# Optimization experiments

Measured on AMD Instinct MI355X. Metric: run time of the kernel, lower is better.

The kernel has to match this reference:

```python
import jax, jax.numpy as jnp
import numpy as np

N_NODES = 50000
N_EDGES = 800000
IN_FEAT = 128
OUT_FEAT = 128


def setup_inputs() -> dict:
    key = jax.random.key(0)
    ks = jax.random.split(key, 12)
    s = lambda fan_in: 1.0 / np.sqrt(fan_in)
    inp = {
        "node_feats": jax.random.normal(ks[0], (N_NODES, IN_FEAT), dtype=jnp.float32),
        "edge_feats": jax.random.normal(ks[1], (N_EDGES, IN_FEAT), dtype=jnp.float32),
        "src": jax.random.randint(ks[2], (N_EDGES,), 0, N_NODES),
        "dst": jax.random.randint(ks[3], (N_EDGES,), 0, N_NODES),
        # mlp1: Linear(2*in -> in), ReLU, Linear(in -> in)
        "W1a": jax.random.uniform(ks[4], (2 * IN_FEAT, IN_FEAT), jnp.float32, -s(2 * IN_FEAT), s(2 * IN_FEAT)),
        "b1a": jnp.zeros((IN_FEAT,), jnp.float32),
        "W1b": jax.random.uniform(ks[5], (IN_FEAT, IN_FEAT), jnp.float32, -s(IN_FEAT), s(IN_FEAT)),
        "b1b": jnp.zeros((IN_FEAT,), jnp.float32),
        # mlp2: Linear(in -> out), ReLU, Linear(out -> out)
        "W2a": jax.random.uniform(ks[6], (IN_FEAT, OUT_FEAT), jnp.float32, -s(IN_FEAT), s(IN_FEAT)),
        "b2a": jnp.zeros((OUT_FEAT,), jnp.float32),
        "W2b": jax.random.uniform(ks[7], (OUT_FEAT, OUT_FEAT), jnp.float32, -s(OUT_FEAT), s(OUT_FEAT)),
        "b2b": jnp.zeros((OUT_FEAT,), jnp.float32),
    }
    return inp


def reference(node_feats, edge_feats, src, dst, W1a, b1a, W1b, b1b, W2a, b2a, W2b, b2b):
    # message: mlp1(cat([h_src, e]))  -> [E, in_feat]
    cat = jnp.concatenate([node_feats[src], edge_feats], axis=1)  # [E, 2*in]
    m = jax.nn.relu(cat @ W1a + b1a) @ W1b + b1b                  # [E, in]
    # reduce: scatter-sum over dst + residual
    agg = jax.ops.segment_sum(m, dst, num_segments=node_feats.shape[0])
    h = agg + node_feats                                          # [N, in]
    # mlp2
    out = jax.nn.relu(h @ W2a + b2a) @ W2b + b2b                  # [N, out]
    return out
```

## Files before the change

### kernel.cpp

```cpp
#include <hip/hip_runtime.h>
#include <hip/hip_bf16.h>

typedef __attribute__((ext_vector_type(8))) short short8;
typedef __attribute__((ext_vector_type(4))) float floatx4;
typedef unsigned short ushort_t;

#define MFMA(a, b, c) __builtin_amdgcn_mfma_f32_16x16x32_bf16((a), (b), (c), 0, 0, 0)

constexpr int N_NODES = 50000;
constexpr int N_EDGES = 800000;
constexpr int EDGE_BLOCKS = N_EDGES / 32;
constexpr int NODE_TILES = (N_NODES + 63) / 64;
constexpr int YS_STRIDE = 136;

__device__ __forceinline__ unsigned short f2b(float x) {
  union { float f; unsigned u; } c; c.f = x;
  unsigned r = c.u + 0x7FFFu + ((c.u >> 16) & 1u);
  return (unsigned short)(r >> 16);
}

__device__ __forceinline__ unsigned pk2(float x, float y) {
  __hip_bfloat162 h = __float22bfloat162_rn(float2{x, y});
  unsigned u; __builtin_memcpy(&u, &h, 4);
  return u;
}

__device__ __forceinline__ short8 mk_frag(const float4 a, const float4 b) {
  union { short8 s; unsigned u[4]; } r;
  r.u[0] = pk2(a.x, a.y); r.u[1] = pk2(a.z, a.w);
  r.u[2] = pk2(b.x, b.y); r.u[3] = pk2(b.z, b.w);
  return r.s;
}

__global__ void prep(const float* __restrict__ W1a, const float* __restrict__ W1b,
                     const float* __restrict__ W2a, const float* __restrict__ W2b,
                     ushort_t* __restrict__ wbuf, float4* __restrict__ agg4) {
  const int t = blockIdx.x * blockDim.x + threadIdx.x;
  const int stride = gridDim.x * blockDim.x;
  const float4 z = {0.f, 0.f, 0.f, 0.f};
  for (int i = t; i < N_NODES * 32; i += stride) agg4[i] = z;

  ushort_t* W1s1 = wbuf;
  ushort_t* W1s2 = wbuf + 32768;
  ushort_t* W2aT = wbuf + 49152;
  ushort_t* W2bT = wbuf + 65536;

  for (int i = t; i < 32768; i += stride) {
    const int j = i & 7, lane = (i >> 3) & 63, fb = i >> 9;
    const int ks = fb >> 3, nt = fb & 7;
    const int k = ks * 32 + (lane >> 4) * 8 + j, n = nt * 16 + (lane & 15);
    W1s1[i] = f2b(W1a[k * 128 + n]);
  }
  for (int i = t; i < 16384; i += stride) {
    const int j = i & 7, lane = (i >> 3) & 63, fb = i >> 9;
    const int ks = fb >> 3, nt = fb & 7;
    const int k = ks * 32 + (lane >> 4) * 8 + j, n = nt * 16 + (lane & 15);
    W1s2[i] = f2b(W1b[k * 128 + n]);
  }
  for (int i = t; i < 16384; i += stride) {
    const int n = i >> 7, k = i & 127;
    W2aT[i] = f2b(W2a[k * 128 + n]);
    W2bT[i] = f2b(W2b[k * 128 + n]);
  }
}

__global__ __launch_bounds__(64, 4) void edge_mlp(
    const float* __restrict__ nf, const float* __restrict__ ef,
    const int* __restrict__ src, const int* __restrict__ dst,
    const float* __restrict__ b1a, const float* __restrict__ b1b,
    const ushort_t* __restrict__ W1s1, const ushort_t* __restrict__ W1s2,
    float* __restrict__ agg) {
  __shared__ __align__(16) ushort_t Ys[32 * YS_STRIDE];

  const int lane = threadIdx.x;
  const int l16 = lane & 15;
  const int quad = lane >> 4;
  const int tb = blockIdx.x * 32;

  const int s0 = src[tb + l16];
  const int s1 = src[tb + 16 + l16];

  floatx4 acc[2][8];
#pragma unroll
  for (int nt = 0; nt < 8; ++nt) {
    const float bz = b1a[nt * 16 + l16];
    acc[0][nt] = (floatx4){bz, bz, bz, bz};
    acc[1][nt] = acc[0][nt];
  }
#pragma unroll
  for (int ks = 0; ks < 8; ++ks) {
    short8 a0, a1;
    if (ks < 4) {
      const float4* p0 = (const float4*)nf + (long)s0 * 32 + ks * 8 + quad * 2;
      const float4* p1 = (const float4*)nf + (long)s1 * 32 + ks * 8 + quad * 2;
      a0 = mk_frag(p0[0], p0[1]);
      a1 = mk_frag(p1[0], p1[1]);
    } else {
      const float4* p0 = (const float4*)ef + (long)(tb + l16) * 32 + (ks - 4) * 8 + quad * 2;
      const float4* p1 = (const float4*)ef + (long)(tb + 16 + l16) * 32 + (ks - 4) * 8 + quad * 2;
      a0 = mk_frag(p0[0], p0[1]);
      a1 = mk_frag(p1[0], p1[1]);
    }
#pragma unroll
    for (int nt = 0; nt < 8; ++nt) {
      const short8 b = *(const short8*)(W1s1 + ((ks * 8 + nt) * 64 + lane) * 8);
      acc[0][nt] = MFMA(a0, b, acc[0][nt]);
      acc[1][nt] = MFMA(a1, b, acc[1][nt]);
    }
  }

#pragma unroll
  for (int mt = 0; mt < 2; ++mt)
#pragma unroll
    for (int nt = 0; nt < 8; ++nt)
#pragma unroll
      for (int r = 0; r < 4; ++r)
        Ys[(mt * 16 + quad * 4 + r) * YS_STRIDE + nt * 16 + l16] =
            f2b(fmaxf(acc[mt][nt][r], 0.f));

  floatx4 acc2[2][8];
#pragma unroll
  for (int nt = 0; nt < 8; ++nt) {
    const float bz = b1b[nt * 16 + l16];
    acc2[0][nt] = (floatx4){bz, bz, bz, bz};
    acc2[1][nt] = acc2[0][nt];
  }
#pragma unroll
  for (int ks = 0; ks < 4; ++ks) {
    const short8 a0 = *(const short8*)(&Ys[l16 * YS_STRIDE + ks * 32 + quad * 8]);
    const short8 a1 = *(const short8*)(&Ys[(16 + l16) * YS_STRIDE + ks * 32 + quad * 8]);
#pragma unroll
    for (int nt = 0; nt < 8; ++nt) {
      const short8 b = *(const short8*)(W1s2 + ((ks * 8 + nt) * 64 + lane) * 8);
      acc2[0][nt] = MFMA(a0, b, acc2[0][nt]);
      acc2[1][nt] = MFMA(a1, b, acc2[1][nt]);
    }
  }

#pragma unroll
  for (int mt = 0; mt < 2; ++mt)
#pragma unroll
    for (int r = 0; r < 4; ++r) {
      const int d = dst[tb + mt * 16 + quad * 4 + r];
      float* base = &agg[(long)d * 128 + l16];
#pragma unroll
      for (int nt = 0; nt < 8; ++nt)
        unsafeAtomicAdd(base + nt * 16, acc2[mt][nt][r]);
    }
}

__global__ __launch_bounds__(256) void node_mlp(
    const float* __restrict__ nf, const float* __restrict__ agg,
    const float* __restrict__ b2a, const float* __restrict__ b2b,
    const ushort_t* __restrict__ W2aT, const ushort_t* __restrict__ W2bT,
    float* __restrict__ out) {
  __shared__ __align__(16) ushort_t Xs[64 * YS_STRIDE];
  __shared__ __align__(16) ushort_t Ys2[64 * YS_STRIDE];

  const int tid = threadIdx.x;
  const int wave = tid >> 6;
  const int lane = tid & 63;
  const int l16 = lane & 15;
  const int quad = lane >> 4;
  const int nbase = wave * 32;
  const int rbase = blockIdx.x * 64;

  short8 bfrA[2][4], bfrB[2][4];
  float biasA[2], biasB[2];
#pragma unroll
  for (int t = 0; t < 2; ++t) {
    const int n = nbase + t * 16 + l16;
#pragma unroll
    for (int ks = 0; ks < 4; ++ks) {
      bfrA[t][ks] = *(const short8*)(W2aT + n * 128 + ks * 32 + quad * 8);
      bfrB[t][ks] = *(const short8*)(W2bT + n * 128 + ks * 32 + quad * 8);
    }
    biasA[t] = b2a[n];
    biasB[t] = b2b[n];
  }

#pragma unroll
  for (int i = 0; i < 8; ++i) {
    const int fidx = tid + 256 * i;
    const int r = fidx >> 5;
    const int c4 = fidx & 31;
    const long gr = min(rbase + r, N_NODES - 1);
    const float4 a = ((const float4*)agg)[gr * 32 + c4];
    const float4 n = ((const float4*)nf)[gr * 32 + c4];
    unsigned* p = (unsigned*)&Xs[r * YS_STRIDE + c4 * 4];
    p[0] = pk2(a.x + n.x, a.y + n.y);
    p[1] = pk2(a.z + n.z, a.w + n.w);
  }
  __syncthreads();

  floatx4 acc[4][2];
#pragma unroll
  for (int mt = 0; mt < 4; ++mt)
#pragma unroll
    for (int t = 0; t < 2; ++t)
      acc[mt][t] = (floatx4){biasA[t], biasA[t], biasA[t], biasA[t]};
#pragma unroll
  for (int ks = 0; ks < 4; ++ks)
#pragma unroll
    for (int mt = 0; mt < 4; ++mt) {
      const short8 a = *(const short8*)(&Xs[(mt * 16 + l16) * YS_STRIDE + ks * 32 + quad * 8]);
      acc[mt][0] = MFMA(a, bfrA[0][ks], acc[mt][0]);
      acc[mt][1] = MFMA(a, bfrA[1][ks], acc[mt][1]);
    }
#pragma unroll
  for (int mt = 0; mt < 4; ++mt)
#pragma unroll
    for (int t = 0; t < 2; ++t)
#pragma unroll
      for (int r = 0; r < 4; ++r) {
        const int row = mt * 16 + quad * 4 + r;
        const int col = nbase + t * 16 + l16;
        Ys2[row * YS_STRIDE + col] = f2b(fmaxf(acc[mt][t][r], 0.f));
      }
  __syncthreads();

  floatx4 acc2[4][2];
#pragma unroll
  for (int mt = 0; mt < 4; ++mt)
#pragma unroll
    for (int t = 0; t < 2; ++t)
      acc2[mt][t] = (floatx4){biasB[t], biasB[t], biasB[t], biasB[t]};
#pragma unroll
  for (int ks = 0; ks < 4; ++ks)
#pragma unroll
    for (int mt = 0; mt < 4; ++mt) {
      const short8 a = *(const short8*)(&Ys2[(mt * 16 + l16) * YS_STRIDE + ks * 32 + quad * 8]);
      acc2[mt][0] = MFMA(a, bfrB[0][ks], acc2[mt][0]);
      acc2[mt][1] = MFMA(a, bfrB[1][ks], acc2[mt][1]);
    }
#pragma unroll
  for (int mt = 0; mt < 4; ++mt)
#pragma unroll
    for (int t = 0; t < 2; ++t)
#pragma unroll
      for (int r = 0; r < 4; ++r) {
        const int row = mt * 16 + quad * 4 + r;
        const int grow = rbase + row;
        if (grow < N_NODES) {
          const int col = nbase + t * 16 + l16;
          out[(long)grow * 128 + col] = acc2[mt][t][r];
        }
      }
}

extern "C" void kernel_launch(void* const* d_in, const int* in_sizes, int n_in,
                              void* d_out, int out_size, void* d_ws, size_t ws_size,
                              hipStream_t stream) {
  const float* nf = (const float*)d_in[0];
  const float* ef = (const float*)d_in[1];
  const int* src = (const int*)d_in[2];
  const int* dst = (const int*)d_in[3];
  const float* W1a = (const float*)d_in[4];
  const float* b1a = (const float*)d_in[5];
  const float* W1b = (const float*)d_in[6];
  const float* b1b = (const float*)d_in[7];
  const float* W2a = (const float*)d_in[8];
  const float* b2a = (const float*)d_in[9];
  const float* W2b = (const float*)d_in[10];
  const float* b2b = (const float*)d_in[11];
  float* out = (float*)d_out;

  char* ws = (char*)d_ws;
  float* agg = (float*)ws;
  ushort_t* wbuf = (ushort_t*)(ws + 25600000);
  const ushort_t* W1s1 = wbuf;
  const ushort_t* W1s2 = wbuf + 32768;
  const ushort_t* W2aT = wbuf + 49152;
  const ushort_t* W2bT = wbuf + 65536;

  prep<<<1024, 256, 0, stream>>>(W1a, W1b, W2a, W2b, wbuf, (float4*)agg);
  edge_mlp<<<EDGE_BLOCKS, 64, 0, stream>>>(nf, ef, src, dst, b1a, b1b, W1s1, W1s2, agg);
  node_mlp<<<NODE_TILES, 256, 0, stream>>>(nf, agg, b2a, b2b, W2aT, W2bT, out);
}
```

Baseline: 1.001 ms.

## Sort edges by destination and pre-reduce messages before atomic scatter

Adds a counting sort of edges by dst (histogram, single-block scan, scatter into a permutation) and has edge_mlp process edges in dst-sorted order. Messages are staged in shared memory and runs of equal dst are summed inside the block, so each run issues one atomic per column instead of one per edge. The sort is meant to cut atomic traffic. In exchange, edge_feats and src are now read as gathers through the permutation rather than streamed, and several extra small kernels run, including a serial one-block scan. The out buffer is reused as scratch for the counts and permutation. Weight fragments are also loaded into registers ahead of each MFMA batch.

Result: faster. 933.8 us (-6.7%).

```diff
diff --git a/kernel.cpp b/kernel.cpp
--- a/kernel.cpp
+++ b/kernel.cpp
@@ -12,6 +12,7 @@
 constexpr int EDGE_BLOCKS = N_EDGES / 32;
 constexpr int NODE_TILES = (N_NODES + 63) / 64;
 constexpr int YS_STRIDE = 136;
+constexpr int MS_STRIDE = 132;
 
 __device__ __forceinline__ unsigned short f2b(float x) {
   union { float f; unsigned u; } c; c.f = x;
@@ -34,11 +35,13 @@
 
 __global__ void prep(const float* __restrict__ W1a, const float* __restrict__ W1b,
                      const float* __restrict__ W2a, const float* __restrict__ W2b,
-                     ushort_t* __restrict__ wbuf, float4* __restrict__ agg4) {
+                     ushort_t* __restrict__ wbuf, float4* __restrict__ agg4,
+                     unsigned* __restrict__ cnt) {
   const int t = blockIdx.x * blockDim.x + threadIdx.x;
   const int stride = gridDim.x * blockDim.x;
   const float4 z = {0.f, 0.f, 0.f, 0.f};
   for (int i = t; i < N_NODES * 32; i += stride) agg4[i] = z;
+  for (int i = t; i < N_NODES; i += stride) cnt[i] = 0u;
 
   ushort_t* W1s1 = wbuf;
   ushort_t* W1s2 = wbuf + 32768;
@@ -64,21 +67,82 @@
   }
 }
 
+__global__ void hist_dst(const int* __restrict__ dst, unsigned* __restrict__ cnt) {
+  int i = blockIdx.x * blockDim.x + threadIdx.x;
+  const int stride = gridDim.x * blockDim.x;
+  for (; i < N_EDGES; i += stride) atomicAdd(&cnt[dst[i]], 1u);
+}
+
+__global__ __launch_bounds__(1024) void scan_cnt(unsigned* __restrict__ cnt) {
+  __shared__ unsigned wsum[16];
+  __shared__ unsigned carry_s;
+  const int tid = threadIdx.x;
+  const int lane = tid & 63, wv = tid >> 6;
+  if (tid == 0) carry_s = 0u;
+  __syncthreads();
+  for (int base = 0; base < N_NODES; base += 1024) {
+    const int i = base + tid;
+    const unsigned v = (i < N_NODES) ? cnt[i] : 0u;
+    unsigned s = v;
+#pragma unroll
+    for (int off = 1; off < 64; off <<= 1) {
+      unsigned t = __shfl_up(s, off);
+      if (lane >= off) s += t;
+    }
+    if (lane == 63) wsum[wv] = s;
+    __syncthreads();
+    if (wv == 0 && lane < 16) {
+      unsigned w = wsum[lane];
+      unsigned sw = w;
+#pragma unroll
+      for (int off = 1; off < 16; off <<= 1) {
+        unsigned t = __shfl_up(sw, off);
+        if (lane >= off) sw += t;
+      }
+      wsum[lane] = sw - w;
+    }
+    __syncthreads();
+    const unsigned excl = s - v + wsum[wv] + carry_s;
+    if (i < N_NODES) cnt[i] = excl;
+    __syncthreads();
+    if (tid == 1023) carry_s = excl + v;
+    __syncthreads();
+  }
+}
+
+__global__ void scatter_idx(const int* __restrict__ dst, unsigned* __restrict__ cnt,
+                            unsigned* __restrict__ perm) {
+  int i = blockIdx.x * blockDim.x + threadIdx.x;
+  const int stride = gridDim.x * blockDim.x;
+  for (; i < N_EDGES; i += stride) {
+    const unsigned pos = atomicAdd(&cnt[dst[i]], 1u);
+    perm[pos] = (unsigned)i;
+  }
+}
+
 __global__ __launch_bounds__(64, 4) void edge_mlp(
     const float* __restrict__ nf, const float* __restrict__ ef,
     const int* __restrict__ src, const int* __restrict__ dst,
+    const unsigned* __restrict__ perm,
     const float* __restrict__ b1a, const float* __restrict__ b1b,
     const ushort_t* __restrict__ W1s1, const ushort_t* __restrict__ W1s2,
     float* __restrict__ agg) {
-  __shared__ __align__(16) ushort_t Ys[32 * YS_STRIDE];
+  __shared__ __align__(16) char smem[32 * MS_STRIDE * 4];
+  ushort_t* Ys = (ushort_t*)smem;
+  float* Ms = (float*)smem;
 
   const int lane = threadIdx.x;
   const int l16 = lane & 15;
   const int quad = lane >> 4;
   const int tb = blockIdx.x * 32;
 
-  const int s0 = src[tb + l16];
-  const int s1 = src[tb + 16 + l16];
+  int dlane = 0;
+  if (lane < 32) dlane = dst[perm[tb + lane]];
+
+  const int e0 = (int)perm[tb + l16];
+  const int e1 = (int)perm[tb + 16 + l16];
+  const int s0 = src[e0];
+  const int s1 = src[e1];
 
   floatx4 acc[2][8];
 #pragma unroll
@@ -96,16 +160,19 @@
       a0 = mk_frag(p0[0], p0[1]);
       a1 = mk_frag(p1[0], p1[1]);
     } else {
-      const float4* p0 = (const float4*)ef + (long)(tb + l16) * 32 + (ks - 4) * 8 + quad * 2;
-      const float4* p1 = (const float4*)ef + (long)(tb + 16 + l16) * 32 + (ks - 4) * 8 + quad * 2;
+      const float4* p0 = (const float4*)ef + (long)e0 * 32 + (ks - 4) * 8 + quad * 2;
+      const float4* p1 = (const float4*)ef + (long)e1 * 32 + (ks - 4) * 8 + quad * 2;
       a0 = mk_frag(p0[0], p0[1]);
       a1 = mk_frag(p1[0], p1[1]);
     }
+    short8 bfr[8];
+#pragma unroll
+    for (int nt = 0; nt < 8; ++nt)
+      bfr[nt] = *(const short8*)(W1s1 + ((ks * 8 + nt) * 64 + lane) * 8);
 #pragma unroll
     for (int nt = 0; nt < 8; ++nt) {
-      const short8 b = *(const short8*)(W1s1 + ((ks * 8 + nt) * 64 + lane) * 8);
-      acc[0][nt] = MFMA(a0, b, acc[0][nt]);
-      acc[1][nt] = MFMA(a1, b, acc[1][nt]);
+      acc[0][nt] = MFMA(a0, bfr[nt], acc[0][nt]);
+      acc[1][nt] = MFMA(a1, bfr[nt], acc[1][nt]);
     }
   }
 
@@ -129,24 +196,39 @@
   for (int ks = 0; ks < 4; ++ks) {
     const short8 a0 = *(const short8*)(&Ys[l16 * YS_STRIDE + ks * 32 + quad * 8]);
     const short8 a1 = *(const short8*)(&Ys[(16 + l16) * YS_STRIDE + ks * 32 + quad * 8]);
+    short8 bfr[8];
+#pragma unroll
+    for (int nt = 0; nt < 8; ++nt)
+      bfr[nt] = *(const short8*)(W1s2 + ((ks * 8 + nt) * 64 + lane) * 8);
 #pragma unroll
     for (int nt = 0; nt < 8; ++nt) {
-      const short8 b = *(const short8*)(W1s2 + ((ks * 8 + nt) * 64 + lane) * 8);
-      acc2[0][nt] = MFMA(a0, b, acc2[0][nt]);
-      acc2[1][nt] = MFMA(a1, b, acc2[1][nt]);
+      acc2[0][nt] = MFMA(a0, bfr[nt], acc2[0][nt]);
+      acc2[1][nt] = MFMA(a1, bfr[nt], acc2[1][nt]);
     }
   }
 
 #pragma unroll
   for (int mt = 0; mt < 2; ++mt)
 #pragma unroll
-    for (int r = 0; r < 4; ++r) {
-      const int d = dst[tb + mt * 16 + quad * 4 + r];
-      float* base = &agg[(long)d * 128 + l16];
-#pragma unroll
-      for (int nt = 0; nt < 8; ++nt)
-        unsafeAtomicAdd(base + nt * 16, acc2[mt][nt][r]);
-    }
+    for (int nt = 0; nt < 8; ++nt)
+#pragma unroll
+      for (int r = 0; r < 4; ++r)
+        Ms[(mt * 16 + quad * 4 + r) * MS_STRIDE + nt * 16 + l16] = acc2[mt][nt][r];
+
+  float a0 = 0.f, a1 = 0.f;
+  int cur = __shfl(dlane, 0);
+  for (int r = 0; r < 32; ++r) {
+    const int d = __shfl(dlane, r);
+    if (d != cur) {
+      unsafeAtomicAdd(&agg[(long)cur * 128 + lane], a0);
+      unsafeAtomicAdd(&agg[(long)cur * 128 + 64 + lane], a1);
+      a0 = 0.f; a1 = 0.f; cur = d;
+    }
+    a0 += Ms[r * MS_STRIDE + lane];
+    a1 += Ms[r * MS_STRIDE + 64 + lane];
+  }
+  unsafeAtomicAdd(&agg[(long)cur * 128 + lane], a0);
+  unsafeAtomicAdd(&agg[(long)cur * 128 + 64 + lane], a1);
 }
 
 __global__ __launch_bounds__(256) void node_mlp(
@@ -273,7 +355,13 @@
   const ushort_t* W2aT = wbuf + 49152;
   const ushort_t* W2bT = wbuf + 65536;
 
-  prep<<<1024, 256, 0, stream>>>(W1a, W1b, W2a, W2b, wbuf, (float4*)agg);
-  edge_mlp<<<EDGE_BLOCKS, 64, 0, stream>>>(nf, ef, src, dst, b1a, b1b, W1s1, W1s2, agg);
+  unsigned* cnt = (unsigned*)out;
+  unsigned* perm = (unsigned*)out + 65536;
+
+  prep<<<1024, 256, 0, stream>>>(W1a, W1b, W2a, W2b, wbuf, (float4*)agg, cnt);
+  hist_dst<<<1024, 256, 0, stream>>>(dst, cnt);
+  scan_cnt<<<1, 1024, 0, stream>>>(cnt);
+  scatter_idx<<<1024, 256, 0, stream>>>(dst, cnt, perm);
+  edge_mlp<<<EDGE_BLOCKS, 64, 0, stream>>>(nf, ef, src, dst, perm, b1a, b1b, W1s1, W1s2, agg);
   node_mlp<<<NODE_TILES, 256, 0, stream>>>(nf, agg, b2a, b2b, W2aT, W2bT, out);
 }
```
